# Performance work log

Measured on AMD Instinct MI355X. Metric: run time of the kernel, lower is better.

## Reference

```python
import jax, jax.numpy as jnp
import numpy as np

D0, D1, D2 = 256, 512, 256  # trials, neurons, time
RANKS = (8, 8, 8)
INIT_W = 1.0 / np.sqrt(sum(RANKS))  # default init_weight for 'uniform'


def _uniform(key, shape):
    # matches torch: 2*(rand-0.5)*init_weight + init_bias(=0)
    return (2.0 * (jax.random.uniform(key, shape, dtype=jnp.float32) - 0.5) * INIT_W)


def setup_inputs() -> dict:
    key = jax.random.key(0)
    k = jax.random.split(key, 6)
    r0, r1, r2 = RANKS
    return {
        # partition 0: [[0],[1,2]] -> vectors [r,D0], [r,D1,D2]
        "v0a": _uniform(k[0], (r0, D0)),
        "v0b": _uniform(k[1], (r0, D1, D2)),
        # partition 1: [[1],[0,2]] -> vectors [r,D1], [r,D0,D2]
        "v1a": _uniform(k[2], (r1, D1)),
        "v1b": _uniform(k[3], (r1, D0, D2)),
        # partition 2: [[2],[0,1]] -> vectors [r,D2], [r,D0,D1]
        "v2a": _uniform(k[4], (r2, D2)),
        "v2b": _uniform(k[5], (r2, D0, D1)),
    }


def reference(v0a, v0b, v1a, v1b, v2a, v2b):
    # construct(): sum over partitions and ranks of outer products, with the
    # per-partition inverse permutation folded into the einsum output subscripts.
    # positive=False -> identity positive_function.
    out = jnp.einsum("ri,rjk->ijk", v0a, v0b)        # partition [[0],[1,2]]
    out = out + jnp.einsum("rj,rik->ijk", v1a, v1b)  # partition [[1],[0,2]]
    out = out + jnp.einsum("rk,rij->ijk", v2a, v2b)  # partition [[2],[0,1]]
    return out  # [D0, D1, D2]
```

## Files before the change

kernel.cpp:

```cpp
#include <hip/hip_runtime.h>


typedef float f4 __attribute__((ext_vector_type(4)));

#define RNK 8
#define DD0 256
#define DD1 512
#define DD2 256
#define TI 8
#define TJ 8
#define KC 128
#define RS 132

__global__ __launch_bounds__(256, 2)
void ptca_kernel(const float* __restrict__ v0a, const float* __restrict__ v0b,
                 const float* __restrict__ v1a, const float* __restrict__ v1b,
                 const float* __restrict__ v2a, const float* __restrict__ v2b,
                 float* __restrict__ out)
{
    __shared__ float sA0[RNK * TJ * RS];
    __shared__ float sA1[RNK * TI * RS];
    __shared__ float sV2[RNK * RS];
    __shared__ float sB2[RNK * TJ * TI];
    __shared__ float sa0[RNK * TI];
    __shared__ float sa1[RNK * TJ];

    const int tid = threadIdx.x;
    const int kl  = tid & 31;
    const int jt  = (tid >> 5) & 3;
    const int it  = tid >> 7;

    const int ib = blockIdx.x * TI;
    const int jb = blockIdx.y * TJ;
    const int kc = blockIdx.z * KC;

#pragma unroll
    for (int q = 0; q < 8; ++q) {
        const int idx = tid + q * 256;
        const int kv = idx & 31;
        const int jl = (idx >> 5) & 7;
        const int r  = idx >> 8;
        *(f4*)(sA0 + (r * TJ + jl) * RS + kv * 4) =
            *(const f4*)(v0b + ((size_t)r * DD1 + jb + jl) * DD2 + kc + kv * 4);
    }
#pragma unroll
    for (int q = 0; q < 8; ++q) {
        const int idx = tid + q * 256;
        const int kv = idx & 31;
        const int il = (idx >> 5) & 7;
        const int r  = idx >> 8;
        *(f4*)(sA1 + (r * TI + il) * RS + kv * 4) =
            *(const f4*)(v1b + ((size_t)r * DD0 + ib + il) * DD2 + kc + kv * 4);
    }
    {
        const int kv = tid & 31;
        const int r  = tid >> 5;
        *(f4*)(sV2 + r * RS + kv * 4) =
            *(const f4*)(v2a + r * DD2 + kc + kv * 4);
    }
#pragma unroll
    for (int q = 0; q < 2; ++q) {
        const int idx = tid + q * 256;
        const int jl = idx & 7;
        const int il = (idx >> 3) & 7;
        const int r  = idx >> 6;
        sB2[(r * TJ + jl) * TI + il] = v2b[((size_t)r * DD0 + ib + il) * DD1 + jb + jl];
    }
    if (tid < 64) {
        sa0[tid] = v0a[(tid >> 3) * DD0 + ib + (tid & 7)];
    } else if (tid < 128) {
        const int t = tid - 64;
        sa1[t] = v1a[(t >> 3) * DD1 + jb + (t & 7)];
    }

    __syncthreads();

    f4 acc[4][2];
#pragma unroll
    for (int di = 0; di < 4; ++di)
#pragma unroll
        for (int dj = 0; dj < 2; ++dj) acc[di][dj] = (f4){0.f, 0.f, 0.f, 0.f};

#pragma unroll
    for (int r = 0; r < RNK; ++r) {
        const f4 f2v = *(const f4*)(sV2 + r * RS + kl * 4);
        const f4 a0q = *(const f4*)(sa0 + r * TI + it * 4);
        f4 f1v[4];
#pragma unroll
        for (int di = 0; di < 4; ++di)
            f1v[di] = *(const f4*)(sA1 + (r * TI + it * 4 + di) * RS + kl * 4);

#pragma unroll
        for (int dj = 0; dj < 2; ++dj) {
            const int j = jt * 2 + dj;
            const f4 f0v = *(const f4*)(sA0 + (r * TJ + j) * RS + kl * 4);
            const f4 s2q = *(const f4*)(sB2 + (r * TJ + j) * TI + it * 4);
            const float a1v = sa1[r * TJ + j];
#pragma unroll
            for (int di = 0; di < 4; ++di)
#pragma unroll
                for (int c = 0; c < 4; ++c)
                    acc[di][dj][c] =
                        __builtin_fmaf(a0q[di], f0v[c],
                        __builtin_fmaf(a1v, f1v[di][c],
                        __builtin_fmaf(s2q[di], f2v[c], acc[di][dj][c])));
        }
    }

#pragma unroll
    for (int di = 0; di < 4; ++di)
#pragma unroll
        for (int dj = 0; dj < 2; ++dj) {
            const size_t off =
                ((size_t)(ib + it * 4 + di) * DD1 + (jb + jt * 2 + dj)) * DD2
                + kc + kl * 4;
            __builtin_nontemporal_store(acc[di][dj], (f4*)(out + off));
        }
}

extern "C" void kernel_launch(void* const* d_in, const int* in_sizes, int n_in,
                              void* d_out, int out_size, void* d_ws, size_t ws_size,
                              hipStream_t stream) {
    const float* v0a = (const float*)d_in[0];
    const float* v0b = (const float*)d_in[1];
    const float* v1a = (const float*)d_in[2];
    const float* v1b = (const float*)d_in[3];
    const float* v2a = (const float*)d_in[4];
    const float* v2b = (const float*)d_in[5];
    float* out = (float*)d_out;

    dim3 grid(DD0 / TI, DD1 / TJ, DD2 / KC);
    ptca_kernel<<<grid, dim3(256), 0, stream>>>(v0a, v0b, v1a, v1b, v2a, v2b, out);
}
```

Measured before the change: 197.2 us.

## Use direct global-to-LDS loads and halve threads with larger per-thread tiles

Global-to-shared staging now uses the global_load_lds builtin, which writes straight into LDS instead of going through registers. The row padding is removed to fit that instruction's contiguous layout. The block drops to 128 threads, each computing a 4x4 (i,j) tile, and v2a is held in registers rather than LDS. This is meant to cut register traffic and instruction count in the load phase and to reuse each LDS read more. In exchange, each block has fewer threads to hide store latency, and the unpadded rows may cause LDS bank conflicts.

```diff
diff --git a/kernel.cpp b/kernel.cpp
--- a/kernel.cpp
+++ b/kernel.cpp
@@ -10,9 +10,20 @@
 #define TI 8
 #define TJ 8
 #define KC 128
-#define RS 132
+#define RS 128
 
-__global__ __launch_bounds__(256, 2)
+__device__ __forceinline__ void gload16(const float* g, float* l) {
+    __builtin_amdgcn_global_load_lds(
+        (const __attribute__((address_space(1))) float*)g,
+        (__attribute__((address_space(3))) float*)l, 16, 0, 0);
+}
+__device__ __forceinline__ void gload4(const float* g, float* l) {
+    __builtin_amdgcn_global_load_lds(
+        (const __attribute__((address_space(1))) float*)g,
+        (__attribute__((address_space(3))) float*)l, 4, 0, 0);
+}
+
+__global__ __launch_bounds__(128, 1)
 void ptca_kernel(const float* __restrict__ v0a, const float* __restrict__ v0b,
                  const float* __restrict__ v1a, const float* __restrict__ v1b,
                  const float* __restrict__ v2a, const float* __restrict__ v2b,
@@ -20,89 +31,90 @@
 {
     __shared__ float sA0[RNK * TJ * RS];
     __shared__ float sA1[RNK * TI * RS];
-    __shared__ float sV2[RNK * RS];
     __shared__ float sB2[RNK * TJ * TI];
     __shared__ float sa0[RNK * TI];
     __shared__ float sa1[RNK * TJ];
 
     const int tid = threadIdx.x;
     const int kl  = tid & 31;
-    const int jt  = (tid >> 5) & 3;
-    const int it  = tid >> 7;
+    const int g   = tid >> 5;
+    const int it  = g & 1;
+    const int jt  = g >> 1;
+    const int wv  = tid >> 6;
 
     const int ib = blockIdx.x * TI;
     const int jb = blockIdx.y * TJ;
     const int kc = blockIdx.z * KC;
 
+    f4 rv2[RNK];
 #pragma unroll
-    for (int q = 0; q < 8; ++q) {
-        const int idx = tid + q * 256;
+    for (int r = 0; r < RNK; ++r)
+        rv2[r] = *(const f4*)(v2a + r * DD2 + kc + kl * 4);
+
+#pragma unroll
+    for (int q = 0; q < 16; ++q) {
+        const int idx = tid + q * 128;
         const int kv = idx & 31;
         const int jl = (idx >> 5) & 7;
         const int r  = idx >> 8;
-        *(f4*)(sA0 + (r * TJ + jl) * RS + kv * 4) =
-            *(const f4*)(v0b + ((size_t)r * DD1 + jb + jl) * DD2 + kc + kv * 4);
+        gload16(v0b + ((size_t)r * DD1 + jb + jl) * DD2 + kc + kv * 4,
+                sA0 + (q * 128 + wv * 64) * 4);
     }
 #pragma unroll
-    for (int q = 0; q < 8; ++q) {
-        const int idx = tid + q * 256;
+    for (int q = 0; q < 16; ++q) {
+        const int idx = tid + q * 128;
         const int kv = idx & 31;
         const int il = (idx >> 5) & 7;
         const int r  = idx >> 8;
-        *(f4*)(sA1 + (r * TI + il) * RS + kv * 4) =
-            *(const f4*)(v1b + ((size_t)r * DD0 + ib + il) * DD2 + kc + kv * 4);
-    }
-    {
-        const int kv = tid & 31;
-        const int r  = tid >> 5;
-        *(f4*)(sV2 + r * RS + kv * 4) =
-            *(const f4*)(v2a + r * DD2 + kc + kv * 4);
+        gload16(v1b + ((size_t)r * DD0 + ib + il) * DD2 + kc + kv * 4,
+                sA1 + (q * 128 + wv * 64) * 4);
     }
 #pragma unroll
-    for (int q = 0; q < 2; ++q) {
-        const int idx = tid + q * 256;
-        const int jl = idx & 7;
-        const int il = (idx >> 3) & 7;
+    for (int q = 0; q < 4; ++q) {
+        const int idx = tid + q * 128;
+        const int il = idx & 7;
+        const int jl = (idx >> 3) & 7;
         const int r  = idx >> 6;
-        sB2[(r * TJ + jl) * TI + il] = v2b[((size_t)r * DD0 + ib + il) * DD1 + jb + jl];
+        gload4(v2b + ((size_t)r * DD0 + ib + il) * DD1 + jb + jl,
+               sB2 + q * 128 + wv * 64);
     }
-    if (tid < 64) {
-        sa0[tid] = v0a[(tid >> 3) * DD0 + ib + (tid & 7)];
-    } else if (tid < 128) {
+    if (wv == 0) {
+        gload4(v0a + (tid >> 3) * DD0 + ib + (tid & 7), sa0);
+    } else {
         const int t = tid - 64;
-        sa1[t] = v1a[(t >> 3) * DD1 + jb + (t & 7)];
+        gload4(v1a + (t >> 3) * DD1 + jb + (t & 7), sa1);
     }
 
     __syncthreads();
 
-    f4 acc[4][2];
+    f4 acc[4][4];
 #pragma unroll
     for (int di = 0; di < 4; ++di)
 #pragma unroll
-        for (int dj = 0; dj < 2; ++dj) acc[di][dj] = (f4){0.f, 0.f, 0.f, 0.f};
+        for (int dj = 0; dj < 4; ++dj) acc[di][dj] = (f4){0.f, 0.f, 0.f, 0.f};
 
 #pragma unroll
     for (int r = 0; r < RNK; ++r) {
-        const f4 f2v = *(const f4*)(sV2 + r * RS + kl * 4);
         const f4 a0q = *(const f4*)(sa0 + r * TI + it * 4);
+        const f4 a1q = *(const f4*)(sa1 + r * TJ + jt * 4);
+        const f4 f2v = rv2[r];
         f4 f1v[4];
 #pragma unroll
         for (int di = 0; di < 4; ++di)
             f1v[di] = *(const f4*)(sA1 + (r * TI + it * 4 + di) * RS + kl * 4);
 
 #pragma unroll
-        for (int dj = 0; dj < 2; ++dj) {
-            const int j = jt * 2 + dj;
+        for (int dj = 0; dj < 4; ++dj) {
+            const int j = jt * 4 + dj;
             const f4 f0v = *(const f4*)(sA0 + (r * TJ + j) * RS + kl * 4);
             const f4 s2q = *(const f4*)(sB2 + (r * TJ + j) * TI + it * 4);
-            const float a1v = sa1[r * TJ + j];
 #pragma unroll
             for (int di = 0; di < 4; ++di)
 #pragma unroll
                 for (int c = 0; c < 4; ++c)
                     acc[di][dj][c] =
                         __builtin_fmaf(a0q[di], f0v[c],
-                        __builtin_fmaf(a1v, f1v[di][c],
+                        __builtin_fmaf(a1q[dj], f1v[di][c],
                         __builtin_fmaf(s2q[di], f2v[c], acc[di][dj][c])));
         }
     }
@@ -110,9 +122,9 @@
 #pragma unroll
     for (int di = 0; di < 4; ++di)
 #pragma unroll
-        for (int dj = 0; dj < 2; ++dj) {
+        for (int dj = 0; dj < 4; ++dj) {
             const size_t off =
-                ((size_t)(ib + it * 4 + di) * DD1 + (jb + jt * 2 + dj)) * DD2
+                ((size_t)(ib + it * 4 + di) * DD1 + (jb + jt * 4 + dj)) * DD2
                 + kc + kl * 4;
             __builtin_nontemporal_store(acc[di][dj], (f4*)(out + off));
         }
@@ -130,5 +142,5 @@
     float* out = (float*)d_out;
 
     dim3 grid(DD0 / TI, DD1 / TJ, DD2 / KC);
-    ptca_kernel<<<grid, dim3(256), 0, stream>>>(v0a, v0b, v1a, v1b, v2a, v2b, out);
+    ptca_kernel<<<grid, dim3(128), 0, stream>>>(v0a, v0b, v1a, v1b, v2a, v2b, out);
 }
```

Result: faster. 192.5 us (median of 2 runs) (-2.4%).
